# Optimization experiments

Hardware: AMD Instinct MI355X
Metric: run time of the kernel (lower is better)

## Reference

```python
import jax, jax.numpy as jnp
import numpy as np
from jax import lax

BN_EPS = 1e-5


def ste_sign(x):
    # binarize to {-1,+1} with straight-through estimator (BNN semantics)
    return x + lax.stop_gradient(jnp.where(x >= 0, 1.0, -1.0).astype(x.dtype) - x)


def _block(x, w, gamma, beta, pool):
    # IRPadding(1,1): pad spatial dims with -1 (binary '0' bit in hardware)
    x = jnp.pad(x, ((0, 0), (0, 0), (1, 1), (1, 1)), constant_values=-1.0)
    # IRConv2dFIN: sign-binarized weights, binary inputs, integer-valued output
    wb = ste_sign(w)
    x = lax.conv_general_dilated(x, wb, window_strides=(1, 1), padding='VALID',
                                 dimension_numbers=('NCHW', 'OIHW', 'NCHW'))
    # IRBatchNorm2d: per-channel batch-stat normalization with affine
    mean = jnp.mean(x, axis=(0, 2, 3), keepdims=True)
    var = jnp.var(x, axis=(0, 2, 3), keepdims=True)
    x = gamma[None, :, None, None] * (x - mean) * lax.rsqrt(var + BN_EPS) + beta[None, :, None, None]
    # Hardtanh then IRCLAP (sign clip to {-1,+1})
    x = jnp.clip(x, -1.0, 1.0)
    x = ste_sign(x)
    if pool:  # MaxPool2d(2,2)
        x = lax.reduce_window(x, -jnp.inf, lax.max, (1, 1, 2, 2), (1, 1, 2, 2), 'VALID')
    return x


def setup_inputs() -> dict:
    key = jax.random.key(0)
    ks = jax.random.split(key, 16)
    B = 256
    x = jnp.where(jax.random.normal(ks[0], (B, 3, 32, 32)) >= 0, 1.0, -1.0).astype(jnp.float32)
    chans = [(128, 3), (256, 128), (256, 256), (256, 256), (128, 256), (128, 128)]
    inp = {'x': x}
    for i, (co, ci) in enumerate(chans):
        n = 3 * 3 * co
        inp[f'w{i}'] = jax.random.normal(ks[1 + i], (co, ci, 3, 3), dtype=jnp.float32) * np.sqrt(2.0 / n)
        inp[f'g{i}'] = jnp.ones((co,), dtype=jnp.float32)
        inp[f'b{i}'] = jnp.zeros((co,), dtype=jnp.float32)
    inp['fc_w'] = jax.random.normal(ks[10], (10, 128 * 4 * 4), dtype=jnp.float32) * 0.01
    inp['fc_b'] = jnp.zeros((10,), dtype=jnp.float32)
    return inp


def reference(x, w0, g0, b0, w1, g1, b1, w2, g2, b2, w3, g3, b3, w4, g4, b4, w5, g5, b5, fc_w, fc_b):
    ws = [w0, w1, w2, w3, w4, w5]
    gs = [g0, g1, g2, g3, g4, g5]
    bs = [b0, b1, b2, b3, b4, b5]
    pools = [False, True, False, True, False, True]
    h = x
    for w, g, b, p in zip(ws, gs, bs, pools):
        h = _block(h, w, g, b, p)
    # flatten (dropout is identity at inference) -> fc
    h = h.reshape(h.shape[0], -1)  # [B, 128*4*4]
    return h @ fc_w.T + fc_b
```

## Files before the change

### kernel.cpp

```cpp
#include <hip/hip_runtime.h>
#include <stdint.h>

typedef unsigned long long ull;
#define BB 256

static const size_t OFF_CONV  = 0;
static const size_t SZ_CONV   = 134217728;
static const size_t OFF_BITSA = 134217728;
static const size_t OFF_BITSB = 138952704;
static const size_t OFF_WB    = 141606912;
static const size_t OFF_S     = 141846528;
static const size_t OFF_SS    = 141852672;
static const size_t OFF_ATHR  = 141864960;
static const size_t OFF_BTHR  = 141877248;
static const size_t OFF_H     = 141889536;
static const size_t WS_NEEDED = 143986688;
static const size_t OFF_XBITS = 100 * 1024 * 1024;


__global__ void zero_stats_k(int* __restrict__ S, ull* __restrict__ SS) {
  int i = blockIdx.x * blockDim.x + threadIdx.x;
  if (i < 6 * 256) { S[i] = 0; SS[i] = 0ull; }
}

__global__ void pack_w_k(const float* __restrict__ w, uint32_t* __restrict__ out,
                         int co, int ci) {
  int K32 = ci >> 5;
  int total = 9 * K32 * co;
  int idx = blockIdx.x * blockDim.x + threadIdx.x;
  if (idx >= total) return;
  int c  = idx % co;
  int tk = idx / co;
  int k  = tk % K32;
  int t  = tk / K32;
  uint32_t word = 0;
  const float* wc = w + (size_t)c * ci * 9 + t;
  for (int j = 0; j < 32; ++j)
    if (wc[(size_t)(k * 32 + j) * 9] >= 0.f) word |= (1u << j);
  out[idx] = word;
}

__global__ void pack_x_k(const float* __restrict__ x, uint32_t* __restrict__ xbits) {
  int idx = blockIdx.x * 256 + threadIdx.x;
  if (idx >= 24576) return;
  const float* xp = x + (size_t)idx * 32;
  uint32_t w = 0;
#pragma unroll
  for (int j = 0; j < 32; ++j) if (xp[j] >= 0.f) w |= (1u << j);
  xbits[idx] = w;
}

__global__ void pack_w0_k(const float* __restrict__ w0, uint32_t* __restrict__ w27) {
  int co = threadIdx.x;
  uint32_t w = 0;
#pragma unroll
  for (int t = 0; t < 27; ++t) if (w0[co * 27 + t] >= 0.f) w |= (1u << t);
  w27[co] = w;
}

__global__ void __launch_bounds__(256) conv0x_k(
    const uint32_t* __restrict__ xbits, const uint32_t* __restrict__ w27,
    short* __restrict__ convout, int* __restrict__ Sg, ull* __restrict__ SSg) {
  int b  = blockIdx.x >> 2;
  int rg = blockIdx.x & 3;
  __shared__ uint32_t a27s[256];
  __shared__ uint32_t wlds[128];
  __shared__ int sS[256], sSS[256];
  int tid = threadIdx.x;
  if (tid < 128) wlds[tid] = w27[tid];

  int p = rg * 256 + tid;
  int y = p >> 5, xx = p & 31;
  const uint32_t* xb = xbits + (size_t)b * 96;
  uint32_t a27 = 0;
#pragma unroll
  for (int c = 0; c < 3; ++c)
#pragma unroll
    for (int kh = 0; kh < 3; ++kh) {
      int iy = y + kh - 1;
      uint32_t r = (iy >= 0 && iy < 32) ? xb[c * 32 + iy] : 0u;
      uint32_t bits3 = (uint32_t)((((uint64_t)r) << 1) >> xx) & 7u;
      a27 |= bits3 << (c * 9 + kh * 3);
    }
  a27s[tid] = a27;
  __syncthreads();

  int co = tid & 127, half = tid >> 7;
  uint32_t wv = wlds[co];
  int S = 0, SS = 0;
  int base = rg * 256 + half * 128;
  short* cb = convout + ((size_t)b * 1024 + base) * 128 + co;
  for (int i = 0; i < 128; ++i) {
    uint32_t a = a27s[half * 128 + i];
    int v = 27 - 2 * __popc(a ^ wv);
    S += v; SS += v * v;
    cb[(size_t)i * 128] = (short)v;
  }
  sS[tid] = S; sSS[tid] = SS;
  __syncthreads();
  if (tid < 128) {
    atomicAdd(&Sg[tid], sS[tid] + sS[tid + 128]);
    atomicAdd(&SSg[tid], (ull)(long long)(sSS[tid] + sSS[tid + 128]));
  }
}

__global__ void finalize_k(const int* __restrict__ S, const ull* __restrict__ SS,
                           int* __restrict__ A, int* __restrict__ B,
                           const float* __restrict__ gamma, const float* __restrict__ beta,
                           int co, int N) {
  int c = threadIdx.x;
  if (c >= co) return;
  double m  = (double)S[c] / (double)N;
  double e2 = (double)SS[c] / (double)N;
  double inv = 1.0 / sqrt(e2 - m * m + 1e-5);
  float gg = gamma[c], bb = beta[c];
  int Ai, Bi;
  if (gg > 0.f) {
    double t = m - (double)bb / ((double)gg * inv);
    t = fmin(fmax(t, -1e6), 1e6);
    Ai = 1;  Bi = (int)ceil(t);
  } else if (gg < 0.f) {
    double t = m - (double)bb / ((double)gg * inv);
    t = fmin(fmax(t, -1e6), 1e6);
    Ai = -1; Bi = -(int)floor(t);
  } else {
    Ai = 0;  Bi = (bb >= 0.f) ? 0 : 1;
  }
  A[c] = Ai; B[c] = Bi;
}

__global__ void binarize_k(const short* __restrict__ conv, int co, int H, int W, int pool,
                           uint32_t* __restrict__ out, const int* __restrict__ A,
                           const int* __restrict__ B, float* __restrict__ hout) {
  __shared__ int As[256], Bs[256];
  int tid = threadIdx.x;
  for (int i = tid; i < co; i += 256) { As[i] = A[i]; Bs[i] = B[i]; }
  __syncthreads();

  int K32 = co >> 5;
  int Ho = pool ? (H >> 1) : H, Wo = pool ? (W >> 1) : W;
  int PH = Ho + 2, PW = Wo + 2;
  int total = BB * K32 * PH * PW;
  int idx = blockIdx.x * 256 + tid;
  if (idx >= total) return;
  int k  = idx % K32;
  int t1 = idx / K32;
  int px = t1 % PW; int t2 = t1 / PW;
  int py = t2 % PH; int b  = t2 / PH;
  uint32_t word = 0;
  if (py >= 1 && py <= Ho && px >= 1 && px <= Wo) {
    int oy = py - 1, ox = px - 1;
    int np = pool ? 2 : 1;
    for (int dy = 0; dy < np; ++dy)
      for (int dx = 0; dx < np; ++dx) {
        int iy = oy * np + dy, ix = ox * np + dx;
        const short* cp = conv + ((size_t)((b * H + iy) * W + ix)) * co + k * 32;
#pragma unroll
        for (int j = 0; j < 32; ++j) {
          int v = cp[j];
          int c = k * 32 + j;
          if (As[c] * v >= Bs[c]) word |= (1u << j);
        }
      }
    if (hout) {
#pragma unroll
      for (int j = 0; j < 32; ++j) {
        int c = k * 32 + j;
        hout[((size_t)(b * 128 + c) * 4 + oy) * 4 + ox] = ((word >> j) & 1) ? 1.f : -1.f;
      }
    }
  }
  out[((size_t)(b * K32 + k) * PH + py) * PW + px] = word;
}

template <int K32>
__global__ void __launch_bounds__(256) conv_xnor_k(
    const uint32_t* __restrict__ act, const uint32_t* __restrict__ wb,
    short* __restrict__ convout, int* __restrict__ Sg, ull* __restrict__ SSg,
    int co, int H, int Ktot) {
  int Hp  = H + 2;
  int T   = H >> 3;
  int cot = co >> 6;
  int TT  = T * T * cot;
  int b   = blockIdx.x / TT;
  int r   = blockIdx.x % TT;
  int ct  = r % cot;
  int tt  = r / cot;
  int ty  = tt / T, tx = tt % T;
  int co_base = ct << 6;

  __shared__ __attribute__((aligned(16))) uint32_t ldsA[K32 * 10 * 12];
  __shared__ __attribute__((aligned(16))) uint32_t ldsB[9 * K32 * 64];
  __shared__ int sS[64];
  __shared__ int sSS[64];

  int tid = threadIdx.x;
  if (tid < 64) { sS[tid] = 0; sSS[tid] = 0; }
  for (int i = tid; i < 9 * K32 * 64; i += 256) {
    int c  = i & 63;
    int tk = i >> 6;
    ldsB[i] = wb[(size_t)tk * co + co_base + c];
  }
  const uint32_t* ab = act + (size_t)b * K32 * Hp * Hp;
  for (int i = tid; i < K32 * 100; i += 256) {
    int k  = i / 100;
    int rr = i % 100;
    int yy = rr / 10, xx = rr % 10;
    ldsA[(k * 10 + yy) * 12 + xx] = ab[(size_t)(k * Hp + ty * 8 + yy) * Hp + tx * 8 + xx];
  }
  __syncthreads();

  int tc   = tid & 15;
  int pgp  = tid >> 4;
  int yrow = pgp >> 1;
  int xg   = pgp & 1;

  int acc[4][4];
#pragma unroll
  for (int i = 0; i < 4; ++i)
#pragma unroll
    for (int j = 0; j < 4; ++j) acc[i][j] = 0;

#pragma unroll 1
  for (int k = 0; k < K32; ++k) {
#pragma unroll
    for (int kh = 0; kh < 3; ++kh) {
      int abase = (k * 10 + yrow + kh) * 12 + xg * 4;
      uint4 a0 = *(const uint4*)&ldsA[abase];
      uint2 a1 = *(const uint2*)&ldsA[abase + 4];
      uint32_t arow[6] = {a0.x, a0.y, a0.z, a0.w, a1.x, a1.y};
#pragma unroll
      for (int kw = 0; kw < 3; ++kw) {
        int t = kh * 3 + kw;
        uint4 bwv = *(const uint4*)&ldsB[(t * K32 + k) * 64 + tc * 4];
        uint32_t bwa[4] = {bwv.x, bwv.y, bwv.z, bwv.w};
#pragma unroll
        for (int pi = 0; pi < 4; ++pi) {
          uint32_t aw = arow[pi + kw];
#pragma unroll
          for (int cj = 0; cj < 4; ++cj)
            acc[pi][cj] += __popc(aw ^ bwa[cj]);
        }
      }
    }
  }

  int vS[4] = {0, 0, 0, 0}, vSS[4] = {0, 0, 0, 0};
  int gy0 = ty * 8 + yrow, gx0 = tx * 8 + xg * 4;
#pragma unroll
  for (int pi = 0; pi < 4; ++pi) {
    short4 vv;
    int v0 = Ktot - 2 * acc[pi][0];
    int v1 = Ktot - 2 * acc[pi][1];
    int v2 = Ktot - 2 * acc[pi][2];
    int v3 = Ktot - 2 * acc[pi][3];
    vS[0] += v0; vSS[0] += v0 * v0;
    vS[1] += v1; vSS[1] += v1 * v1;
    vS[2] += v2; vSS[2] += v2 * v2;
    vS[3] += v3; vSS[3] += v3 * v3;
    vv.x = (short)v0; vv.y = (short)v1; vv.z = (short)v2; vv.w = (short)v3;
    size_t obase = ((size_t)(b * H + gy0) * H + (gx0 + pi)) * co + co_base + tc * 4;
    *(short4*)&convout[obase] = vv;
  }
#pragma unroll
  for (int cj = 0; cj < 4; ++cj) {
    atomicAdd(&sS[tc * 4 + cj], vS[cj]);
    atomicAdd(&sSS[tc * 4 + cj], vSS[cj]);
  }
  __syncthreads();
  if (tid < 64) {
    atomicAdd(&Sg[co_base + tid], sS[tid]);
    atomicAdd(&SSg[co_base + tid], (ull)(long long)sSS[tid]);
  }
}

__global__ void fc_k(const float* __restrict__ h, const float* __restrict__ fcw,
                     const float* __restrict__ fcb, float* __restrict__ out) {
  int b = blockIdx.x;
  int tid = threadIdx.x;
  int j = tid & 15;
  int chunk = tid >> 4;
  __shared__ float red[16][17];
  float acc = 0.f;
  if (j < 10) {
    const float* hp = h + (size_t)b * 2048 + chunk * 128;
    const float* wp = fcw + (size_t)j * 2048 + chunk * 128;
    for (int i = 0; i < 128; ++i) acc += hp[i] * wp[i];
  }
  red[chunk][j] = acc;
  __syncthreads();
  if (tid < 10) {
    float s = fcb[tid];
    for (int c = 0; c < 16; ++c) s += red[c][tid];
    out[b * 10 + tid] = s;
  }
}


extern "C" void kernel_launch(void* const* d_in, const int* in_sizes, int n_in,
                              void* d_out, int out_size, void* d_ws, size_t ws_size,
                              hipStream_t stream) {
  (void)in_sizes; (void)n_in; (void)out_size;
  if (ws_size < WS_NEEDED) return;

  const float* x = (const float*)d_in[0];
  const float* w[6]; const float* g[6]; const float* bt[6];
  for (int i = 0; i < 6; ++i) {
    w[i]  = (const float*)d_in[1 + 3 * i];
    g[i]  = (const float*)d_in[2 + 3 * i];
    bt[i] = (const float*)d_in[3 + 3 * i];
  }
  const float* fcw = (const float*)d_in[19];
  const float* fcb = (const float*)d_in[20];

  char* ws = (char*)d_ws;
  short*     convout = (short*)(ws + OFF_CONV);
  uint32_t*  bitsA   = (uint32_t*)(ws + OFF_BITSA);
  uint32_t*  bitsB   = (uint32_t*)(ws + OFF_BITSB);
  uint32_t*  wbits   = (uint32_t*)(ws + OFF_WB);
  int*       Sg      = (int*)(ws + OFF_S);
  ull*       SSg     = (ull*)(ws + OFF_SS);
  int*       Athr    = (int*)(ws + OFF_ATHR);
  int*       Bthr    = (int*)(ws + OFF_BTHR);
  float*     hbuf    = (float*)(ws + OFF_H);
  uint32_t*  xbits   = (uint32_t*)(ws + OFF_XBITS);
  uint32_t*  w27     = xbits + 24576;
  float*     out     = (float*)d_out;

  zero_stats_k<<<6, 256, 0, stream>>>(Sg, SSg);

  pack_w_k<<<(9 * 4 * 256 + 255) / 256, 256, 0, stream>>>(w[1], wbits + 0,     256, 128);
  pack_w_k<<<(9 * 8 * 256 + 255) / 256, 256, 0, stream>>>(w[2], wbits + 9216,  256, 256);
  pack_w_k<<<(9 * 8 * 256 + 255) / 256, 256, 0, stream>>>(w[3], wbits + 27648, 256, 256);
  pack_w_k<<<(9 * 8 * 128 + 255) / 256, 256, 0, stream>>>(w[4], wbits + 46080, 128, 256);
  pack_w_k<<<(9 * 4 * 128 + 255) / 256, 256, 0, stream>>>(w[5], wbits + 55296, 128, 128);
  pack_x_k<<<96, 256, 0, stream>>>(x, xbits);
  pack_w0_k<<<1, 128, 0, stream>>>(w[0], w27);

  conv0x_k<<<256 * 4, 256, 0, stream>>>(xbits, w27, convout, Sg, SSg);
  finalize_k<<<1, 256, 0, stream>>>(Sg, SSg, Athr, Bthr, g[0], bt[0], 128, 262144);
  binarize_k<<<(256 * 4 * 34 * 34 + 255) / 256, 256, 0, stream>>>(
      convout, 128, 32, 32, 0, bitsA, Athr, Bthr, nullptr);

  conv_xnor_k<4><<<256 * 16 * 4, 256, 0, stream>>>(bitsA, wbits + 0, convout,
                                                   Sg + 256, SSg + 256, 256, 32, 1152);
  finalize_k<<<1, 256, 0, stream>>>(Sg + 256, SSg + 256, Athr + 256, Bthr + 256, g[1], bt[1], 256, 262144);
  binarize_k<<<(256 * 8 * 18 * 18 + 255) / 256, 256, 0, stream>>>(
      convout, 256, 32, 32, 1, bitsB, Athr + 256, Bthr + 256, nullptr);

  conv_xnor_k<8><<<256 * 4 * 4, 256, 0, stream>>>(bitsB, wbits + 9216, convout,
                                                  Sg + 512, SSg + 512, 256, 16, 2304);
  finalize_k<<<1, 256, 0, stream>>>(Sg + 512, SSg + 512, Athr + 512, Bthr + 512, g[2], bt[2], 256, 65536);
  binarize_k<<<(256 * 8 * 18 * 18 + 255) / 256, 256, 0, stream>>>(
      convout, 256, 16, 16, 0, bitsA, Athr + 512, Bthr + 512, nullptr);

  conv_xnor_k<8><<<256 * 4 * 4, 256, 0, stream>>>(bitsA, wbits + 27648, convout,
                                                  Sg + 768, SSg + 768, 256, 16, 2304);
  finalize_k<<<1, 256, 0, stream>>>(Sg + 768, SSg + 768, Athr + 768, Bthr + 768, g[3], bt[3], 256, 65536);
  binarize_k<<<(256 * 8 * 10 * 10 + 255) / 256, 256, 0, stream>>>(
      convout, 256, 16, 16, 1, bitsB, Athr + 768, Bthr + 768, nullptr);

  conv_xnor_k<8><<<256 * 1 * 2, 256, 0, stream>>>(bitsB, wbits + 46080, convout,
                                                  Sg + 1024, SSg + 1024, 128, 8, 2304);
  finalize_k<<<1, 256, 0, stream>>>(Sg + 1024, SSg + 1024, Athr + 1024, Bthr + 1024, g[4], bt[4], 128, 16384);
  binarize_k<<<(256 * 4 * 10 * 10 + 255) / 256, 256, 0, stream>>>(
      convout, 128, 8, 8, 0, bitsA, Athr + 1024, Bthr + 1024, nullptr);

  conv_xnor_k<4><<<256 * 1 * 2, 256, 0, stream>>>(bitsA, wbits + 55296, convout,
                                                  Sg + 1280, SSg + 1280, 128, 8, 1152);
  finalize_k<<<1, 256, 0, stream>>>(Sg + 1280, SSg + 1280, Athr + 1280, Bthr + 1280, g[5], bt[5], 128, 16384);
  binarize_k<<<(256 * 4 * 6 * 6 + 255) / 256, 256, 0, stream>>>(
      convout, 128, 8, 8, 1, bitsB, Athr + 1280, Bthr + 1280, hbuf);

  fc_k<<<256, 256, 0, stream>>>(hbuf, fcw, fcb, out);
}
```

Baseline: 575.8 us.

## Replace XNOR-popcount convs in layers 1-3 with int8 MFMA implicit GEMM

Layers 1-3 now store binarized activations as ±1 int8 in a padded NHWC layout and run the convolutions as implicit GEMM on the int8 MFMA instruction (32x32x32), using swizzled LDS tiles and prepacked weight fragments. Conv outputs are written in fragment order, and a new binarize kernel reads them through LDS, fusing BN thresholding and max-pool. Layer 1 is split into two 128-channel halves to limit workspace, and extra memsets initialise the padding borders. The goal is to move the bulk of the work from scalar popcount to the matrix cores, at the cost of 8x more activation traffic than bit-packed storage.

```diff
diff --git a/kernel.cpp b/kernel.cpp
--- a/kernel.cpp
+++ b/kernel.cpp
@@ -2,20 +2,26 @@
 #include <stdint.h>
 
 typedef unsigned long long ull;
+typedef int i32x4 __attribute__((ext_vector_type(4)));
+typedef int i32x16 __attribute__((ext_vector_type(16)));
 #define BB 256
 
 static const size_t OFF_CONV  = 0;
-static const size_t SZ_CONV   = 134217728;
-static const size_t OFF_BITSA = 134217728;
-static const size_t OFF_BITSB = 138952704;
-static const size_t OFF_WB    = 141606912;
-static const size_t OFF_S     = 141846528;
-static const size_t OFF_SS    = 141852672;
-static const size_t OFF_ATHR  = 141864960;
-static const size_t OFF_BTHR  = 141877248;
-static const size_t OFF_H     = 141889536;
-static const size_t WS_NEEDED = 143986688;
-static const size_t OFF_XBITS = 100 * 1024 * 1024;
+static const size_t OFF_ACT1  = 67108864;
+static const size_t OFF_ACT2  = 104988672;
+static const size_t OFF_BITS4 = 126222336;
+static const size_t OFF_BITS5 = 127041536;
+static const size_t OFF_WBPC  = 127451136;
+static const size_t OFF_WPK   = 127506432;
+static const size_t OFF_S     = 128980992;
+static const size_t OFF_SS    = 128987136;
+static const size_t OFF_ATHR  = 128999424;
+static const size_t OFF_BTHR  = 129005568;
+static const size_t OFF_H     = 129011712;
+static const size_t OFF_XB    = 131108864;
+static const size_t WS_NEEDED = 131207680;
+
+#define SWZA(o) ((o) ^ (((((o) >> 7) ^ ((o) >> 10)) & 7) << 4))
 
 
 __global__ void zero_stats_k(int* __restrict__ S, ull* __restrict__ SS) {
@@ -38,6 +44,33 @@
   for (int j = 0; j < 32; ++j)
     if (wc[(size_t)(k * 32 + j) * 9] >= 0.f) word |= (1u << j);
   out[idx] = word;
+}
+
+__global__ void pack_wmfma_k(const float* __restrict__ w, signed char* __restrict__ out,
+                             int co, int ci) {
+  int KT = ci >> 5;
+  int total = (co >> 5) * 9 * KT * 64;
+  int idx = blockIdx.x * blockDim.x + threadIdx.x;
+  if (idx >= total) return;
+  int l   = idx & 63;
+  int ctk = idx >> 6;
+  int kt  = ctk % KT; int tmp = ctk / KT;
+  int t   = tmp % 9;  int ct  = tmp / 9;
+  int co_ = ct * 32 + (l & 31);
+  int ci0 = kt * 32 + (l >> 5) * 16;
+  const float* wp = w + ((size_t)co_ * ci + ci0) * 9 + t;
+  int dw[4];
+#pragma unroll
+  for (int jj = 0; jj < 4; ++jj) {
+    uint32_t d = 0;
+#pragma unroll
+    for (int bb = 0; bb < 4; ++bb) {
+      float f = wp[(size_t)(jj * 4 + bb) * 9];
+      d |= ((f >= 0.f) ? 0x01u : 0xFFu) << (8 * bb);
+    }
+    dw[jj] = (int)d;
+  }
+  *(i32x4*)(out + (size_t)idx * 16) = *(i32x4*)&dw[0];
 }
 
 __global__ void pack_x_k(const float* __restrict__ x, uint32_t* __restrict__ xbits) {
@@ -130,8 +163,9 @@
 }
 
 __global__ void binarize_k(const short* __restrict__ conv, int co, int H, int W, int pool,
-                           uint32_t* __restrict__ out, const int* __restrict__ A,
-                           const int* __restrict__ B, float* __restrict__ hout) {
+                           uint32_t* __restrict__ out_bits, signed char* __restrict__ out8,
+                           const int* __restrict__ A, const int* __restrict__ B,
+                           float* __restrict__ hout) {
   __shared__ int As[256], Bs[256];
   int tid = threadIdx.x;
   for (int i = tid; i < co; i += 256) { As[i] = A[i]; Bs[i] = B[i]; }
@@ -170,7 +204,214 @@
       }
     }
   }
-  out[((size_t)(b * K32 + k) * PH + py) * PW + px] = word;
+  if (out_bits)
+    out_bits[((size_t)(b * K32 + k) * PH + py) * PW + px] = word;
+  if (out8) {
+    int dw[8];
+#pragma unroll
+    for (int jj = 0; jj < 8; ++jj) {
+      uint32_t d = 0;
+#pragma unroll
+      for (int bb = 0; bb < 4; ++bb)
+        d |= (((word >> (jj * 4 + bb)) & 1) ? 0x01u : 0xFFu) << (8 * bb);
+      dw[jj] = (int)d;
+    }
+    signed char* p = out8 + (((size_t)(b * PH + py)) * PW + px) * (size_t)co + k * 32;
+    *(i32x4*)p = *(i32x4*)&dw[0];
+    *(i32x4*)(p + 16) = *(i32x4*)&dw[4];
+  }
+}
+
+template <int CI, int W, int CO_BLK>
+__global__ __launch_bounds__(256, 2) void conv_mfma_k(
+    const signed char* __restrict__ act, const i32x4* __restrict__ wpk,
+    short* __restrict__ convout, int* __restrict__ Sg, ull* __restrict__ SSg) {
+  constexpr int KT = CI / 32;
+  constexpr int PW = W + 2;
+  constexpr int TR = 32 / W;
+  constexpr int ROWS_BLK = 4 * TR;
+  constexpr int NBY = W / ROWS_BLK;
+  constexpr int AROWS = ROWS_BLK + 2;
+  constexpr int ABYTES = AROWS * PW * CI;
+  constexpr int NSTEP = 9 * KT;
+  constexpr int NT = CO_BLK / 64;
+
+  __shared__ __attribute__((aligned(16))) char ldsA[ABYTES];
+
+  int tid = threadIdx.x;
+  int b = blockIdx.x / NBY, blk_y = blockIdx.x % NBY;
+  int y0 = blk_y * ROWS_BLK;
+
+  const signed char* src = act + ((size_t)b * (W + 2) + y0) * PW * CI;
+  for (int o = tid * 16; o < ABYTES; o += 4096) {
+    i32x4 v = *(const i32x4*)(src + o);
+    *(i32x4*)(ldsA + SWZA(o)) = v;
+  }
+  __syncthreads();
+
+  int l = tid & 63, w = tid >> 6;
+  int wm = w & 1, wn = w >> 1;
+  int r = l & 31, khalf = l >> 5;
+  int px = (TR == 1) ? r : (r & 15);
+
+  int inv[2];
+#pragma unroll
+  for (int m = 0; m < 2; ++m) {
+    int ti = wm * 2 + m;
+    int row = (TR == 1) ? ti : (ti * 2 + (r >> 4));
+    inv[m] = (row * PW + px) * CI + khalf * 16;
+  }
+  const i32x4* wl = wpk + l;
+
+  i32x16 acc[2][NT];
+#pragma unroll
+  for (int m = 0; m < 2; ++m)
+#pragma unroll
+    for (int n = 0; n < NT; ++n)
+#pragma unroll
+      for (int q = 0; q < 16; ++q) acc[m][n][q] = 0;
+
+  auto LOADS = [&](int s, i32x4 (&a)[2], i32x4 (&bf)[NT]) {
+    int t = s / KT, kt = s % KT;
+    int soff = ((t / 3) * PW + (t % 3)) * CI + kt * 32;
+#pragma unroll
+    for (int m = 0; m < 2; ++m) {
+      int o = inv[m] + soff;
+      o = SWZA(o);
+      a[m] = *(const i32x4*)(ldsA + o);
+    }
+#pragma unroll
+    for (int n = 0; n < NT; ++n)
+      bf[n] = wl[(size_t)(((wn * NT + n) * 9 + t) * KT + kt) * 64];
+  };
+  auto MFMAALL = [&](i32x4 (&a)[2], i32x4 (&bf)[NT]) {
+#pragma unroll
+    for (int m = 0; m < 2; ++m)
+#pragma unroll
+      for (int n = 0; n < NT; ++n)
+        acc[m][n] = __builtin_amdgcn_mfma_i32_32x32x32_i8(a[m], bf[n], acc[m][n], 0, 0, 0);
+  };
+
+  i32x4 aA[2], bA[NT], aB[2], bB[NT];
+  LOADS(0, aA, bA);
+  int s = 0;
+  for (; s + 2 < NSTEP; s += 2) {
+    LOADS(s + 1, aB, bB);
+    MFMAALL(aA, bA);
+    LOADS(s + 2, aA, bA);
+    MFMAALL(aB, bB);
+  }
+  LOADS(NSTEP - 1, aB, bB);
+  MFMAALL(aA, bA);
+  MFMAALL(aB, bB);
+
+#pragma unroll
+  for (int n = 0; n < NT; ++n) {
+    int s1 = 0, s2 = 0;
+#pragma unroll
+    for (int m = 0; m < 2; ++m) {
+      int ti = wm * 2 + m;
+      i32x16 v = acc[m][n];
+      int pk[8];
+#pragma unroll
+      for (int q = 0; q < 8; ++q) {
+        int v0 = v[2 * q], v1 = v[2 * q + 1];
+        s1 += v0 + v1; s2 += v0 * v0 + v1 * v1;
+        pk[q] = (v0 & 0xffff) | (v1 << 16);
+      }
+      int fragLocal = ti * (2 * NT) + wn * NT + n;
+      size_t baseS = (((size_t)blockIdx.x * (8 * NT) + fragLocal) * 64 + l) * 16;
+      *(i32x4*)(convout + baseS) = *(i32x4*)&pk[0];
+      *(i32x4*)(convout + baseS + 8) = *(i32x4*)&pk[4];
+    }
+    s1 += __shfl_xor(s1, 32);
+    s2 += __shfl_xor(s2, 32);
+    if (l < 32) {
+      int ch = wn * (NT * 32) + n * 32 + l;
+      atomicAdd(&Sg[ch], s1);
+      atomicAdd(&SSg[ch], (ull)(long long)s2);
+    }
+  }
+}
+
+template <int CO_BLK, int W, int POOL, int OUT_BITS, int OUTP>
+__global__ __launch_bounds__(256) void binarize_frag_k(
+    const short* __restrict__ convout, signed char* __restrict__ out8,
+    uint32_t* __restrict__ out_bits, const int* __restrict__ Ath,
+    const int* __restrict__ Bth, int co_base) {
+  constexpr int TR = 32 / W;
+  constexpr int ROWS_BLK = 4 * TR;
+  constexpr int NBY = W / ROWS_BLK;
+  constexpr int K32B = CO_BLK / 32;
+  constexpr int NT = CO_BLK / 64;
+  constexpr int Wout = POOL ? W / 2 : W;
+  constexpr int HoutB = POOL ? ROWS_BLK / 2 : ROWS_BLK;
+  constexpr int WORDS = HoutB * Wout * K32B;
+  constexpr int NP = POOL ? 2 : 1;
+  constexpr int LBYTES = 128 * CO_BLK * 2;
+
+  __shared__ __attribute__((aligned(16))) char ldsC[LBYTES];
+  int tid = threadIdx.x;
+  int b = blockIdx.x / NBY, blk_y = blockIdx.x % NBY;
+
+  const char* src = (const char*)(convout + (size_t)blockIdx.x * (128 * CO_BLK));
+  for (int o = tid * 16; o < LBYTES; o += 4096) {
+    i32x4 v = *(const i32x4*)(src + o);
+    int so = o ^ (((o >> 11) & 7) << 4);
+    *(i32x4*)(ldsC + so) = v;
+  }
+  __syncthreads();
+
+  for (int widx = tid; widx < WORDS; widx += 256) {
+    int k = widx % K32B, opx = widx / K32B;
+    int oy = opx / Wout, ox = opx % Wout;
+    int wn = k / NT, n = k % NT;
+    int bases[NP * NP];
+#pragma unroll
+    for (int dy = 0; dy < NP; ++dy)
+#pragma unroll
+      for (int dx = 0; dx < NP; ++dx) {
+        int yl = POOL ? oy * 2 + dy : oy;
+        int x  = POOL ? ox * 2 + dx : ox;
+        int ti = yl / TR;
+        int rr = (TR == 1) ? x : ((yl & 1) * 16 + x);
+        int hi = (rr >> 2) & 1, q = (rr & 3) + 4 * (rr >> 3);
+        int fragLocal = ti * K32B + wn * NT + n;
+        bases[dy * NP + dx] = ((fragLocal * 64 + hi * 32) * 16 + q) * 2;
+      }
+    uint32_t word = 0;
+    for (int j = 0; j < 32; ++j) {
+      int c = k * 32 + j;
+      int Aj = Ath[c], Bj = Bth[c];
+      int mx = -0x7fffffff;
+#pragma unroll
+      for (int p2 = 0; p2 < NP * NP; ++p2) {
+        int bo = bases[p2] + j * 32;
+        bo ^= ((bo >> 11) & 7) << 4;
+        int v = *(const short*)(ldsC + bo);
+        int av = Aj * v;
+        mx = (av > mx) ? av : mx;
+      }
+      if (mx >= Bj) word |= (1u << j);
+    }
+    int gy = blk_y * HoutB + oy, gx = ox;
+    if (OUT_BITS) {
+      out_bits[(((size_t)b * K32B + k) * OUTP + 1 + gy) * OUTP + 1 + gx] = word;
+    } else {
+      size_t a0 = (((size_t)b * OUTP + (1 + gy)) * OUTP + (1 + gx)) * 256 + co_base + k * 32;
+      int dw[8];
+#pragma unroll
+      for (int jj = 0; jj < 8; ++jj) {
+        uint32_t d = 0;
+#pragma unroll
+        for (int bb = 0; bb < 4; ++bb)
+          d |= (((word >> (jj * 4 + bb)) & 1) ? 0x01u : 0xFFu) << (8 * bb);
+        dw[jj] = (int)d;
+      }
+      *(i32x4*)(out8 + a0) = *(i32x4*)&dw[0];
+      *(i32x4*)(out8 + a0 + 16) = *(i32x4*)&dw[4];
+    }
+  }
 }
 
 template <int K32>
@@ -314,63 +555,76 @@
   const float* fcb = (const float*)d_in[20];
 
   char* ws = (char*)d_ws;
-  short*     convout = (short*)(ws + OFF_CONV);
-  uint32_t*  bitsA   = (uint32_t*)(ws + OFF_BITSA);
-  uint32_t*  bitsB   = (uint32_t*)(ws + OFF_BITSB);
-  uint32_t*  wbits   = (uint32_t*)(ws + OFF_WB);
-  int*       Sg      = (int*)(ws + OFF_S);
-  ull*       SSg     = (ull*)(ws + OFF_SS);
-  int*       Athr    = (int*)(ws + OFF_ATHR);
-  int*       Bthr    = (int*)(ws + OFF_BTHR);
-  float*     hbuf    = (float*)(ws + OFF_H);
-  uint32_t*  xbits   = (uint32_t*)(ws + OFF_XBITS);
-  uint32_t*  w27     = xbits + 24576;
-  float*     out     = (float*)d_out;
+  short*        convout = (short*)(ws + OFF_CONV);
+  signed char*  act1    = (signed char*)(ws + OFF_ACT1);
+  signed char*  act2    = (signed char*)(ws + OFF_ACT2);
+  uint32_t*     bits4   = (uint32_t*)(ws + OFF_BITS4);
+  uint32_t*     bits5   = (uint32_t*)(ws + OFF_BITS5);
+  uint32_t*     wbpc    = (uint32_t*)(ws + OFF_WBPC);
+  signed char*  wpkc    = (signed char*)(ws + OFF_WPK);
+  int*          Sg      = (int*)(ws + OFF_S);
+  ull*          SSg     = (ull*)(ws + OFF_SS);
+  int*          Athr    = (int*)(ws + OFF_ATHR);
+  int*          Bthr    = (int*)(ws + OFF_BTHR);
+  float*        hbuf    = (float*)(ws + OFF_H);
+  uint32_t*     xbits   = (uint32_t*)(ws + OFF_XB);
+  uint32_t*     w27     = xbits + 24576;
+  float*        out     = (float*)d_out;
+
+  const i32x4* wpk1 = (const i32x4*)wpkc;
+  const i32x4* wpk2 = wpk1 + 294912 / 16;
+  const i32x4* wpk3 = wpk1 + 884736 / 16;
 
   zero_stats_k<<<6, 256, 0, stream>>>(Sg, SSg);
 
-  pack_w_k<<<(9 * 4 * 256 + 255) / 256, 256, 0, stream>>>(w[1], wbits + 0,     256, 128);
-  pack_w_k<<<(9 * 8 * 256 + 255) / 256, 256, 0, stream>>>(w[2], wbits + 9216,  256, 256);
-  pack_w_k<<<(9 * 8 * 256 + 255) / 256, 256, 0, stream>>>(w[3], wbits + 27648, 256, 256);
-  pack_w_k<<<(9 * 8 * 128 + 255) / 256, 256, 0, stream>>>(w[4], wbits + 46080, 128, 256);
-  pack_w_k<<<(9 * 4 * 128 + 255) / 256, 256, 0, stream>>>(w[5], wbits + 55296, 128, 128);
+  pack_w_k<<<36, 256, 0, stream>>>(w[4], wbpc, 128, 256);
+  pack_w_k<<<18, 256, 0, stream>>>(w[5], wbpc + 9216, 128, 128);
+  pack_wmfma_k<<<72, 256, 0, stream>>>(w[1], wpkc, 256, 128);
+  pack_wmfma_k<<<144, 256, 0, stream>>>(w[2], wpkc + 294912, 256, 256);
+  pack_wmfma_k<<<144, 256, 0, stream>>>(w[3], wpkc + 884736, 256, 256);
   pack_x_k<<<96, 256, 0, stream>>>(x, xbits);
   pack_w0_k<<<1, 128, 0, stream>>>(w[0], w27);
+
+  hipMemsetAsync(act2, 0xFF, 21233664, stream);
+  hipMemsetAsync(bits4, 0x00, 819200, stream);
 
   conv0x_k<<<256 * 4, 256, 0, stream>>>(xbits, w27, convout, Sg, SSg);
   finalize_k<<<1, 256, 0, stream>>>(Sg, SSg, Athr, Bthr, g[0], bt[0], 128, 262144);
   binarize_k<<<(256 * 4 * 34 * 34 + 255) / 256, 256, 0, stream>>>(
-      convout, 128, 32, 32, 0, bitsA, Athr, Bthr, nullptr);
-
-  conv_xnor_k<4><<<256 * 16 * 4, 256, 0, stream>>>(bitsA, wbits + 0, convout,
-                                                   Sg + 256, SSg + 256, 256, 32, 1152);
-  finalize_k<<<1, 256, 0, stream>>>(Sg + 256, SSg + 256, Athr + 256, Bthr + 256, g[1], bt[1], 256, 262144);
-  binarize_k<<<(256 * 8 * 18 * 18 + 255) / 256, 256, 0, stream>>>(
-      convout, 256, 32, 32, 1, bitsB, Athr + 256, Bthr + 256, nullptr);
-
-  conv_xnor_k<8><<<256 * 4 * 4, 256, 0, stream>>>(bitsB, wbits + 9216, convout,
-                                                  Sg + 512, SSg + 512, 256, 16, 2304);
+      convout, 128, 32, 32, 0, nullptr, act1, Athr, Bthr, nullptr);
+
+  conv_mfma_k<128, 32, 128><<<2048, 256, 0, stream>>>(act1, wpk1, convout, Sg + 256, SSg + 256);
+  finalize_k<<<1, 256, 0, stream>>>(Sg + 256, SSg + 256, Athr + 256, Bthr + 256, g[1], bt[1], 128, 262144);
+  binarize_frag_k<128, 32, 1, 0, 18><<<2048, 256, 0, stream>>>(
+      convout, act2, nullptr, Athr + 256, Bthr + 256, 0);
+
+  conv_mfma_k<128, 32, 128><<<2048, 256, 0, stream>>>(act1, wpk1 + 9216, convout, Sg + 384, SSg + 384);
+  finalize_k<<<1, 256, 0, stream>>>(Sg + 384, SSg + 384, Athr + 384, Bthr + 384, g[1] + 128, bt[1] + 128, 128, 262144);
+  hipMemsetAsync(act1, 0xFF, 21233664, stream);
+  binarize_frag_k<128, 32, 1, 0, 18><<<2048, 256, 0, stream>>>(
+      convout, act2, nullptr, Athr + 384, Bthr + 384, 128);
+
+  conv_mfma_k<256, 16, 256><<<512, 256, 0, stream>>>(act2, wpk2, convout, Sg + 512, SSg + 512);
   finalize_k<<<1, 256, 0, stream>>>(Sg + 512, SSg + 512, Athr + 512, Bthr + 512, g[2], bt[2], 256, 65536);
-  binarize_k<<<(256 * 8 * 18 * 18 + 255) / 256, 256, 0, stream>>>(
-      convout, 256, 16, 16, 0, bitsA, Athr + 512, Bthr + 512, nullptr);
-
-  conv_xnor_k<8><<<256 * 4 * 4, 256, 0, stream>>>(bitsA, wbits + 27648, convout,
-                                                  Sg + 768, SSg + 768, 256, 16, 2304);
+  binarize_frag_k<256, 16, 0, 0, 18><<<512, 256, 0, stream>>>(
+      convout, act1, nullptr, Athr + 512, Bthr + 512, 0);
+
+  conv_mfma_k<256, 16, 256><<<512, 256, 0, stream>>>(act1, wpk3, convout, Sg + 768, SSg + 768);
   finalize_k<<<1, 256, 0, stream>>>(Sg + 768, SSg + 768, Athr + 768, Bthr + 768, g[3], bt[3], 256, 65536);
-  binarize_k<<<(256 * 8 * 10 * 10 + 255) / 256, 256, 0, stream>>>(
-      convout, 256, 16, 16, 1, bitsB, Athr + 768, Bthr + 768, nullptr);
-
-  conv_xnor_k<8><<<256 * 1 * 2, 256, 0, stream>>>(bitsB, wbits + 46080, convout,
-                                                  Sg + 1024, SSg + 1024, 128, 8, 2304);
+  binarize_frag_k<256, 16, 1, 1, 10><<<512, 256, 0, stream>>>(
+      convout, nullptr, bits4, Athr + 768, Bthr + 768, 0);
+
+  conv_xnor_k<8><<<256 * 2, 256, 0, stream>>>(bits4, wbpc, convout,
+                                              Sg + 1024, SSg + 1024, 128, 8, 2304);
   finalize_k<<<1, 256, 0, stream>>>(Sg + 1024, SSg + 1024, Athr + 1024, Bthr + 1024, g[4], bt[4], 128, 16384);
   binarize_k<<<(256 * 4 * 10 * 10 + 255) / 256, 256, 0, stream>>>(
-      convout, 128, 8, 8, 0, bitsA, Athr + 1024, Bthr + 1024, nullptr);
-
-  conv_xnor_k<4><<<256 * 1 * 2, 256, 0, stream>>>(bitsA, wbits + 55296, convout,
-                                                  Sg + 1280, SSg + 1280, 128, 8, 1152);
+      convout, 128, 8, 8, 0, bits5, nullptr, Athr + 1024, Bthr + 1024, nullptr);
+
+  conv_xnor_k<4><<<256 * 2, 256, 0, stream>>>(bits5, wbpc + 9216, convout,
+                                              Sg + 1280, SSg + 1280, 128, 8, 1152);
   finalize_k<<<1, 256, 0, stream>>>(Sg + 1280, SSg + 1280, Athr + 1280, Bthr + 1280, g[5], bt[5], 128, 16384);
   binarize_k<<<(256 * 4 * 6 * 6 + 255) / 256, 256, 0, stream>>>(
-      convout, 128, 8, 8, 1, bitsB, Athr + 1280, Bthr + 1280, hbuf);
+      convout, 128, 8, 8, 1, bits4, nullptr, Athr + 1280, Bthr + 1280, hbuf);
 
   fc_k<<<256, 256, 0, stream>>>(hbuf, fcw, fcb, out);
 }
```

New measurement: 648.3 us. 1.13x slower.
